# Performance work log

Measured on AMD Instinct MI355X. Metric: run time of the kernel, lower is better.

## Reference

```python
import jax, jax.numpy as jnp
import numpy as np

N = 50000       # nodes
E = 800000      # edges
IN_DIM = 256    # input_dim
HEADS = 4
CH = 32         # per-head channels (hidden_dim; conv3 uses latent_dim//heads = 32 too)
HC = HEADS * CH # 128
ED = 32         # edge_dims


def setup_inputs():
    key = jax.random.key(0)
    ks = iter(jax.random.split(key, 64))
    def nrm(shape):
        return jax.random.normal(next(ks), shape, dtype=jnp.float32) * 0.05
    inp = {}
    inp["x"] = nrm((N, IN_DIM))
    inp["edge_index"] = jax.random.randint(next(ks), (2, E), 0, N)
    inp["attr"] = nrm((E, ED))
    for l, ind in ((1, IN_DIM), (2, HC), (3, HC)):
        inp[f"Wq{l}"] = nrm((ind, HC)); inp[f"bq{l}"] = jnp.zeros((HC,), jnp.float32)
        inp[f"Wk{l}"] = nrm((ind, HC)); inp[f"bk{l}"] = jnp.zeros((HC,), jnp.float32)
        inp[f"Wv{l}"] = nrm((ind, HC)); inp[f"bv{l}"] = jnp.zeros((HC,), jnp.float32)
        inp[f"We{l}"] = nrm((ED, HC))  # lin_edge has no bias in PyG TransformerConv
        inp[f"Ws{l}"] = nrm((ind, HC)); inp[f"bs{l}"] = jnp.zeros((HC,), jnp.float32)
    inp["g1"] = jnp.ones((HC,), jnp.float32); inp["be1"] = jnp.zeros((HC,), jnp.float32)
    inp["g2"] = jnp.ones((HC,), jnp.float32); inp["be2"] = jnp.zeros((HC,), jnp.float32)
    return inp


def _transformer_conv(x, src, dst, attr, Wq, bq, Wk, bk, Wv, bv, We, Ws, bs):
    # PyG TransformerConv, concat=True, root_weight=True, beta=False, dropout=0 (eval).
    q = (x @ Wq + bq).reshape(-1, HEADS, CH)   # [N,H,C] (queries at dst)
    k = (x @ Wk + bk).reshape(-1, HEADS, CH)
    v = (x @ Wv + bv).reshape(-1, HEADS, CH)
    e = (attr @ We).reshape(-1, HEADS, CH)     # [E,H,C]
    kj = k[src] + e                            # edge-conditioned keys  [E,H,C]
    vj = v[src] + e                            # edge-conditioned values [E,H,C]
    alpha = jnp.einsum('ehc,ehc->eh', q[dst], kj) / np.sqrt(CH).astype(np.float32)
    # segment softmax over incoming edges per destination node, per head
    amax = jax.ops.segment_max(alpha, dst, num_segments=N)          # [N,H]
    amax = jnp.where(jnp.isfinite(amax), amax, 0.0)                 # nodes with no edges
    ex = jnp.exp(alpha - amax[dst])                                 # [E,H]
    den = jax.ops.segment_sum(ex, dst, num_segments=N)              # [N,H]
    a = ex / (den[dst] + 1e-16)                                     # [E,H]
    out = jax.ops.segment_sum(a[..., None] * vj, dst, num_segments=N)  # [N,H,C]
    out = out.reshape(-1, HC) + (x @ Ws + bs)                       # + root skip
    return out, a


def _layernorm(x, g, b):
    m = x.mean(-1, keepdims=True)
    v = x.var(-1, keepdims=True)
    return (x - m) / jnp.sqrt(v + 1e-5) * g + b


def reference(x, edge_index, attr,
              Wq1, bq1, Wk1, bk1, Wv1, bv1, We1, Ws1, bs1,
              Wq2, bq2, Wk2, bk2, Wv2, bv2, We2, Ws2, bs2,
              Wq3, bq3, Wk3, bk3, Wv3, bv3, We3, Ws3, bs3,
              g1, be1, g2, be2):
    src, dst = edge_index[0], edge_index[1]
    h, a1 = _transformer_conv(x, src, dst, attr, Wq1, bq1, Wk1, bk1, Wv1, bv1, We1, Ws1, bs1)
    h = jax.nn.relu(_layernorm(h, g1, be1))   # dropout is identity in eval
    h, a2 = _transformer_conv(h, src, dst, attr, Wq2, bq2, Wk2, bk2, Wv2, bv2, We2, Ws2, bs2)
    h = jax.nn.relu(_layernorm(h, g2, be2))
    h, a3 = _transformer_conv(h, src, dst, attr, Wq3, bq3, Wk3, bk3, Wv3, bv3, We3, Ws3, bs3)
    return (h, a1, a2, a3)
```

## Files before the change

kernel.cpp:

```cpp
#include <hip/hip_runtime.h>
#include <math.h>

#define N_NODES 50000
#define E_EDGES 800000
#define HC 128
#define ED 32
#define SCH 64
#define SCHSZ 782

typedef __attribute__((ext_vector_type(8))) short bf16x8;
typedef __attribute__((ext_vector_type(4))) float f32x4;
typedef unsigned short ushort_t;

__device__ __forceinline__ ushort_t f2bf(float f){
    unsigned u = __float_as_uint(f);
    return (ushort_t)((u + 0x7FFFu + ((u >> 16) & 1u)) >> 16);
}
__device__ __forceinline__ float bflo(unsigned u){ return __uint_as_float(u << 16); }
__device__ __forceinline__ float bfhi(unsigned u){ return __uint_as_float(u & 0xffff0000u); }

__device__ __forceinline__ int weidx(int c, int d){
    return c * 40 + (((((d >> 2) + ((c >> 3) & 7)) & 7)) << 2) + (d & 3);
}


__global__ void hist_kernel(const int* __restrict__ dst, int* __restrict__ cnt, int n_edges){
    int e = blockIdx.x * blockDim.x + threadIdx.x;
    if (e < n_edges) atomicAdd(&cnt[dst[e]], 1);
}

__global__ __launch_bounds__(256) void chunk_hist_kernel(const int* __restrict__ cnt,
                                                         int* __restrict__ chist){
    __shared__ int hist[64];
    const int t = threadIdx.x, b = blockIdx.x;
    if (t < 64) hist[t] = 0;
    __syncthreads();
    const int base = b * SCHSZ;
    const int lim = min(base + SCHSZ, N_NODES);
    for (int i = base + t; i < lim; i += 256){
        int d = cnt[i]; if (d > 63) d = 63;
        atomicAdd(&hist[d], 1);
    }
    __syncthreads();
    if (t < 64) chist[b * 64 + t] = hist[t];
}

__global__ __launch_bounds__(1024) void scan_sort_kernel(
    const int* __restrict__ cnt, int* __restrict__ rowptr,
    int* __restrict__ cursor, const int* __restrict__ chist, int* __restrict__ cbase)
{
    __shared__ int part[1024];
    __shared__ int ch[SCH * 64];
    __shared__ int binbase[64];
    const int t = threadIdx.x;
    const int CH = (N_NODES + 1023) / 1024;
    const int base = t * CH;
    int s = 0;
    for (int i = 0; i < CH; i++){
        int idx = base + i;
        if (idx < N_NODES) s += cnt[idx];
    }
    part[t] = s;
    __syncthreads();
    for (int off = 1; off < 1024; off <<= 1){
        int v = (t >= off) ? part[t - off] : 0;
        __syncthreads();
        part[t] += v;
        __syncthreads();
    }
    int off = (t == 0) ? 0 : part[t - 1];
    for (int i = 0; i < CH; i++){
        int idx = base + i;
        if (idx < N_NODES){
            int c = cnt[idx];
            rowptr[idx] = off;
            cursor[idx] = off;
            off += c;
        }
    }
    if (t == 1023) rowptr[N_NODES] = part[1023];

    for (int i = t; i < SCH * 64; i += 1024) ch[i] = chist[i];
    __syncthreads();
    if (t < 64){
        int tot = 0;
        for (int c = 0; c < SCH; c++) tot += ch[c * 64 + t];
        binbase[t] = tot;
    }
    __syncthreads();
    if (t == 0){
        int acc = 0;
        for (int b = 0; b < 64; b++){ int v = binbase[b]; binbase[b] = acc; acc += v; }
    }
    __syncthreads();
    for (int i = t; i < SCH * 64; i += 1024){
        int c = i >> 6, d = i & 63;
        int acc = binbase[d];
        for (int c2 = 0; c2 < c; c2++) acc += ch[c2 * 64 + d];
        cbase[i] = acc;
    }
}

__global__ __launch_bounds__(256) void scatter_kernel(
    const int* __restrict__ src, const int* __restrict__ dst,
    int* __restrict__ cursor, int2* __restrict__ es, int n_edges,
    const int* __restrict__ cnt, const int* __restrict__ cbase, int* __restrict__ norder)
{
    __shared__ int cur[64];
    const int b = blockIdx.x, t = threadIdx.x;
    const bool sorter = (b < SCH);
    if (sorter && t < 64) cur[t] = cbase[b * 64 + t];
    int e = b * 256 + t;
    if (e < n_edges){
        int d = dst[e];
        int pos = atomicAdd(&cursor[d], 1);
        es[pos] = make_int2(e, src[e]);
    }
    if (sorter){
        __syncthreads();
        const int base = b * SCHSZ;
        const int lim = min(base + SCHSZ, N_NODES);
        for (int i = base + t; i < lim; i += 256){
            int d = cnt[i]; if (d > 63) d = 63;
            int pos = atomicAdd(&cur[d], 1);
            norder[pos] = i;
        }
    }
}

__device__ __forceinline__ void pack_item(const float* __restrict__ Wq, const float* __restrict__ Wk,
                                          const float* __restrict__ Wv, const float* __restrict__ Ws,
                                          const float* __restrict__ We, ushort_t* __restrict__ Bp,
                                          int K, int item){
    int n = item % 640, k = item / 640;
    float val;
    if (n < 512){
        const float* W = (n < 128) ? Wq : (n < 256) ? Wk : (n < 384) ? Wv : Ws;
        val = W[k * HC + (n & 127)];
    } else {
        int col = n - 512, h5 = (col >> 5) * 32, d = col & 31;
        float acc = 0.f;
        for (int c = 0; c < 32; c++)
            acc = fmaf(Wq[k * HC + h5 + c], We[d * HC + h5 + c], acc);
        val = acc;
    }
    Bp[(((size_t)(k >> 3)) * 640 + n) * 8 + (k & 7)] = f2bf(val);
}

#define T_S0 12800000
#define T_S1 16000000
#define T_S2 16163840
#define T_S3 16245760
#define T_S4 16327680
#define T_S5 16328064

__global__ __launch_bounds__(256) void tail_kernel(
    const float* __restrict__ attr, const int2* __restrict__ es,
    const float* __restrict__ x, int perm_mode,
    ushort_t* __restrict__ attr_bf, ushort_t* __restrict__ Xbf,
    const float* __restrict__ Wq0, const float* __restrict__ bq0, const float* __restrict__ Wk0,
    const float* __restrict__ Wv0, const float* __restrict__ Ws0, const float* __restrict__ We0,
    const float* __restrict__ Wq1, const float* __restrict__ bq1, const float* __restrict__ Wk1,
    const float* __restrict__ Wv1, const float* __restrict__ Ws1, const float* __restrict__ We1,
    const float* __restrict__ Wq2, const float* __restrict__ bq2, const float* __restrict__ Wk2,
    const float* __restrict__ Wv2, const float* __restrict__ Ws2, const float* __restrict__ We2,
    ushort_t* __restrict__ Bp0, ushort_t* __restrict__ Bp1, ushort_t* __restrict__ Bp2,
    float* __restrict__ qwb3)
{
    const int stride = gridDim.x * blockDim.x;
    for (int gi = blockIdx.x * blockDim.x + threadIdx.x; gi < T_S5; gi += stride){
        if (gi < T_S0){
            if (perm_mode){
                int grp = gi >> 4, lane = gi & 15;
                int e = es[grp].x;
                const float2 v = *(const float2*)&attr[(size_t)e * ED + lane * 2];
                unsigned r = (unsigned)f2bf(v.x) | ((unsigned)f2bf(v.y) << 16);
                ((unsigned*)attr_bf)[(size_t)grp * (ED / 2) + lane] = r;
            }
        } else if (gi < T_S1){
            int i = gi - T_S0;
            float4 v = ((const float4*)x)[i];
            ushort_t r0 = f2bf(v.x), r1 = f2bf(v.y), r2 = f2bf(v.z), r3 = f2bf(v.w);
            ((ushort4*)Xbf)[i] = make_ushort4(r0, r1, r2, r3);
        } else if (gi < T_S2){
            pack_item(Wq0, Wk0, Wv0, Ws0, We0, Bp0, 256, gi - T_S1);
        } else if (gi < T_S3){
            pack_item(Wq1, Wk1, Wv1, Ws1, We1, Bp1, 128, gi - T_S2);
        } else if (gi < T_S4){
            pack_item(Wq2, Wk2, Wv2, Ws2, We2, Bp2, 128, gi - T_S3);
        } else {
            int f = gi - T_S4;
            int l = f >> 7, t2 = f & 127;
            const float* bq = (l == 0) ? bq0 : (l == 1) ? bq1 : bq2;
            const float* We = (l == 0) ? We0 : (l == 1) ? We1 : We2;
            int h5 = (t2 >> 5) * 32, d = t2 & 31;
            float acc = 0.f;
            for (int c = 0; c < 32; c++)
                acc = fmaf(bq[h5 + c], We[d * HC + h5 + c], acc);
            qwb3[l * HC + t2] = acc;
        }
    }
}

template<int K>
__global__ __launch_bounds__(320) void gemm_mfma(
    const ushort_t* __restrict__ Xbf, const ushort_t* __restrict__ Bpack,
    const float* __restrict__ b0, const float* __restrict__ b1,
    const float* __restrict__ b2, const float* __restrict__ b3,
    const float* __restrict__ b4,
    float* __restrict__ Yq, ushort_t* __restrict__ Ykbf,
    ushort_t* __restrict__ Yvbf, float* __restrict__ Ys,
    float* __restrict__ Yw, int M)
{
    const int w = threadIdx.x >> 6;
    const int lane = threadIdx.x & 63;
    const int q = lane >> 4, nn = lane & 15;
    const int row0 = blockIdx.x * 32;

    f32x4 acc[2][8];
    #pragma unroll
    for (int mt = 0; mt < 2; mt++)
        #pragma unroll
        for (int nt = 0; nt < 8; nt++)
            acc[mt][nt] = (f32x4){0.f, 0.f, 0.f, 0.f};

    const int r0 = row0 + nn;
    const int r1 = row0 + 16 + nn;
    const bf16x8 zf = (bf16x8){0,0,0,0,0,0,0,0};

    #pragma unroll
    for (int kc = 0; kc < K / 32; kc++){
        bf16x8 a0 = (r0 < M) ? *(const bf16x8*)&Xbf[(size_t)r0 * K + kc * 32 + q * 8] : zf;
        bf16x8 a1 = (r1 < M) ? *(const bf16x8*)&Xbf[(size_t)r1 * K + kc * 32 + q * 8] : zf;
        bf16x8 b[8];
        #pragma unroll
        for (int nt = 0; nt < 8; nt++){
            int n = w * 128 + nt * 16 + nn;
            b[nt] = *(const bf16x8*)&Bpack[(((size_t)(kc * 4 + q)) * 640 + n) * 8];
        }
        #pragma unroll
        for (int nt = 0; nt < 8; nt++){
            acc[0][nt] = __builtin_amdgcn_mfma_f32_16x16x32_bf16(a0, b[nt], acc[0][nt], 0, 0, 0);
            acc[1][nt] = __builtin_amdgcn_mfma_f32_16x16x32_bf16(a1, b[nt], acc[1][nt], 0, 0, 0);
        }
    }

    const float scale = (w == 0 || w == 4) ? 0.17677669529663687f : 1.f;
    const float* bias = (w == 0) ? b0 : (w == 1) ? b1 : (w == 2) ? b2 : (w == 3) ? b3 : b4;

    if (w == 1 || w == 2){
        ushort_t* Yb = (w == 1) ? Ykbf : Yvbf;
        #pragma unroll
        for (int nt = 0; nt < 8; nt++){
            int col = nt * 16 + nn;
            float bval = bias[col];
            #pragma unroll
            for (int mt = 0; mt < 2; mt++){
                #pragma unroll
                for (int r = 0; r < 4; r++){
                    int row = row0 + mt * 16 + q * 4 + r;
                    if (row < M) Yb[(size_t)row * HC + col] = f2bf(acc[mt][nt][r] + bval);
                }
            }
        }
    } else {
        float* Y = (w == 0) ? Yq : (w == 3) ? Ys : Yw;
        #pragma unroll
        for (int nt = 0; nt < 8; nt++){
            int col = nt * 16 + nn;
            float bval = bias[col];
            #pragma unroll
            for (int mt = 0; mt < 2; mt++){
                #pragma unroll
                for (int r = 0; r < 4; r++){
                    int row = row0 + mt * 16 + q * 4 + r;
                    if (row < M) Y[(size_t)row * HC + col] = (acc[mt][nt][r] + bval) * scale;
                }
            }
        }
    }
}

__device__ __forceinline__ float dot16s(const uint4 kk, const uint4 aa,
                                        const float4 qA, const float4 qB,
                                        const float4 wA, const float4 wB){
    float pa =            bflo(kk.x) * qA.x;
    pa = fmaf(bfhi(kk.x), qA.y, pa);
    pa = fmaf(bflo(kk.y), qA.z, pa);
    pa = fmaf(bfhi(kk.y), qA.w, pa);
    pa = fmaf(bflo(aa.x), wA.x, pa);
    pa = fmaf(bfhi(aa.x), wA.y, pa);
    pa = fmaf(bflo(aa.y), wA.z, pa);
    pa = fmaf(bfhi(aa.y), wA.w, pa);
    float pb =            bflo(kk.z) * qB.x;
    pb = fmaf(bfhi(kk.z), qB.y, pb);
    pb = fmaf(bflo(kk.w), qB.z, pb);
    pb = fmaf(bfhi(kk.w), qB.w, pb);
    pb = fmaf(bflo(aa.z), wB.x, pb);
    pb = fmaf(bfhi(aa.z), wB.y, pb);
    pb = fmaf(bflo(aa.w), wB.z, pb);
    pb = fmaf(bfhi(aa.w), wB.w, pb);
    return pa + pb;
}

__device__ __forceinline__ uint4 packrow(const float* p){
    float4 x = *(const float4*)p;
    float4 y = *(const float4*)(p + 4);
    uint4 r;
    r.x = (unsigned)f2bf(x.x) | ((unsigned)f2bf(x.y) << 16);
    r.y = (unsigned)f2bf(x.z) | ((unsigned)f2bf(x.w) << 16);
    r.z = (unsigned)f2bf(y.x) | ((unsigned)f2bf(y.y) << 16);
    r.w = (unsigned)f2bf(y.z) | ((unsigned)f2bf(y.w) << 16);
    return r;
}

__global__ __launch_bounds__(256) void fused_attn_kernel(
    const float* __restrict__ qs, const float* __restrict__ qw,
    const ushort_t* __restrict__ kb, const ushort_t* __restrict__ vb,
    const float* __restrict__ skip, const float* __restrict__ We,
    const float* __restrict__ attr, const ushort_t* __restrict__ attr_bf, int perm_mode,
    const int* __restrict__ rowptr, const int2* __restrict__ es,
    const int* __restrict__ norder,
    float* __restrict__ acsr, float* __restrict__ a_out,
    const float* __restrict__ g, const float* __restrict__ be,
    float* __restrict__ out_f32, ushort_t* __restrict__ out_bf, int apply_ln)
{
    __shared__ float WeT[5120];
    __shared__ float SL[2304];
    const int t = threadIdx.x;
    for (int idx = t; idx < ED * HC; idx += 256){
        int d = idx >> 7, c = idx & 127;
        WeT[weidx(c, d)] = We[idx];
    }
    __syncthreads();

    const int lane = t & 63, wvi = t >> 6;
    const int qq = lane >> 4, li = lane & 15;
    const int h = li >> 2, jj = li & 3;
    const int gq = blockIdx.x * 16 + wvi * 4 + qq;
    if (gq >= N_NODES) return;
    const int n = norder[gq];
    const int ch = h * 32 + jj * 8;
    const size_t nrow = (size_t)n * HC + ch;

    const float4 qA = *(const float4*)&qs[nrow];
    const float4 qB = *(const float4*)&qs[nrow + 4];
    const float4 wA = *(const float4*)&qw[nrow];
    const float4 wB = *(const float4*)&qw[nrow + 4];
    const float4 skA = *(const float4*)&skip[nrow];
    const float4 skB = *(const float4*)&skip[nrow + 4];

    const int beg = rowptr[n], end = rowptr[n + 1];
    float m = -1e30f, s = 0.f;
    float acc[8] = {0,0,0,0,0,0,0,0};
    float S[8]   = {0,0,0,0,0,0,0,0};

    for (int i = beg; i < end; i += 4){
        const int cnt = end - i;
        uint4 kk[4], vv[4], aa[4];
        #pragma unroll
        for (int b = 0; b < 4; b++){
            kk[b] = (uint4){0,0,0,0}; vv[b] = (uint4){0,0,0,0}; aa[b] = (uint4){0,0,0,0};
            if (b < cnt){
                const int2 e = es[i + b];
                kk[b] = *(const uint4*)&kb[(size_t)e.y * HC + ch];
                vv[b] = *(const uint4*)&vb[(size_t)e.y * HC + ch];
                if (perm_mode)
                    aa[b] = *(const uint4*)&attr_bf[(size_t)(i + b) * ED + jj * 8];
                else
                    aa[b] = packrow(&attr[(size_t)e.x * ED + jj * 8]);
            }
        }
        float al[4];
        #pragma unroll
        for (int b = 0; b < 4; b++){
            float p = dot16s(kk[b], aa[b], qA, qB, wA, wB);
            p += __shfl_xor(p, 1);
            p += __shfl_xor(p, 2);
            al[b] = (b < cnt) ? p : -1e38f;
        }
        if (jj == 0){
            #pragma unroll
            for (int b = 0; b < 4; b++)
                if (b < cnt) acsr[(size_t)(i + b) * 4 + h] = al[b];
        }
        const float mn = fmaxf(fmaxf(m, fmaxf(al[0], al[1])), fmaxf(al[2], al[3]));
        const float sc = __expf(m - mn);
        m = mn;
        const float w0 = __expf(al[0] - mn);
        const float w1 = __expf(al[1] - mn);
        const float w2 = __expf(al[2] - mn);
        const float w3 = __expf(al[3] - mn);
        s = fmaf(s, sc, (w0 + w1) + (w2 + w3));
        acc[0] = fmaf(acc[0], sc, fmaf(w0, bflo(vv[0].x), fmaf(w1, bflo(vv[1].x), fmaf(w2, bflo(vv[2].x), w3 * bflo(vv[3].x)))));
        acc[1] = fmaf(acc[1], sc, fmaf(w0, bfhi(vv[0].x), fmaf(w1, bfhi(vv[1].x), fmaf(w2, bfhi(vv[2].x), w3 * bfhi(vv[3].x)))));
        acc[2] = fmaf(acc[2], sc, fmaf(w0, bflo(vv[0].y), fmaf(w1, bflo(vv[1].y), fmaf(w2, bflo(vv[2].y), w3 * bflo(vv[3].y)))));
        acc[3] = fmaf(acc[3], sc, fmaf(w0, bfhi(vv[0].y), fmaf(w1, bfhi(vv[1].y), fmaf(w2, bfhi(vv[2].y), w3 * bfhi(vv[3].y)))));
        acc[4] = fmaf(acc[4], sc, fmaf(w0, bflo(vv[0].z), fmaf(w1, bflo(vv[1].z), fmaf(w2, bflo(vv[2].z), w3 * bflo(vv[3].z)))));
        acc[5] = fmaf(acc[5], sc, fmaf(w0, bfhi(vv[0].z), fmaf(w1, bfhi(vv[1].z), fmaf(w2, bfhi(vv[2].z), w3 * bfhi(vv[3].z)))));
        acc[6] = fmaf(acc[6], sc, fmaf(w0, bflo(vv[0].w), fmaf(w1, bflo(vv[1].w), fmaf(w2, bflo(vv[2].w), w3 * bflo(vv[3].w)))));
        acc[7] = fmaf(acc[7], sc, fmaf(w0, bfhi(vv[0].w), fmaf(w1, bfhi(vv[1].w), fmaf(w2, bfhi(vv[2].w), w3 * bfhi(vv[3].w)))));
        S[0] = fmaf(S[0], sc, fmaf(w0, bflo(aa[0].x), fmaf(w1, bflo(aa[1].x), fmaf(w2, bflo(aa[2].x), w3 * bflo(aa[3].x)))));
        S[1] = fmaf(S[1], sc, fmaf(w0, bfhi(aa[0].x), fmaf(w1, bfhi(aa[1].x), fmaf(w2, bfhi(aa[2].x), w3 * bfhi(aa[3].x)))));
        S[2] = fmaf(S[2], sc, fmaf(w0, bflo(aa[0].y), fmaf(w1, bflo(aa[1].y), fmaf(w2, bflo(aa[2].y), w3 * bflo(aa[3].y)))));
        S[3] = fmaf(S[3], sc, fmaf(w0, bfhi(aa[0].y), fmaf(w1, bfhi(aa[1].y), fmaf(w2, bfhi(aa[2].y), w3 * bfhi(aa[3].y)))));
        S[4] = fmaf(S[4], sc, fmaf(w0, bflo(aa[0].z), fmaf(w1, bflo(aa[1].z), fmaf(w2, bflo(aa[2].z), w3 * bflo(aa[3].z)))));
        S[5] = fmaf(S[5], sc, fmaf(w0, bfhi(aa[0].z), fmaf(w1, bfhi(aa[1].z), fmaf(w2, bfhi(aa[2].z), w3 * bfhi(aa[3].z)))));
        S[6] = fmaf(S[6], sc, fmaf(w0, bflo(aa[0].w), fmaf(w1, bflo(aa[1].w), fmaf(w2, bflo(aa[2].w), w3 * bflo(aa[3].w)))));
        S[7] = fmaf(S[7], sc, fmaf(w0, bfhi(aa[0].w), fmaf(w1, bfhi(aa[1].w), fmaf(w2, bfhi(aa[2].w), w3 * bfhi(aa[3].w)))));
    }

    const int nl = wvi * 4 + qq;
    const int sbase = nl * 144;
    const int hsk = h * 36;
    *(float4*)&SL[sbase + hsk + jj * 8]     = make_float4(S[0], S[1], S[2], S[3]);
    *(float4*)&SL[sbase + hsk + jj * 8 + 4] = make_float4(S[4], S[5], S[6], S[7]);
    asm volatile("" ::: "memory");
    float E[8] = {0,0,0,0,0,0,0,0};
    #pragma unroll
    for (int d4 = 0; d4 < 8; d4++){
        const float4 sv = *(const float4*)&SL[sbase + hsk + d4 * 4];
        #pragma unroll
        for (int r = 0; r < 8; r++){
            const float4 wv = *(const float4*)&WeT[weidx(ch + r, d4 * 4)];
            E[r] = fmaf(sv.x, wv.x, fmaf(sv.y, wv.y, fmaf(sv.z, wv.z, fmaf(sv.w, wv.w, E[r]))));
        }
    }

    const float inv = 1.f / (s + 1e-16f);
    float o[8];
    o[0] = (acc[0] + E[0]) * inv + skA.x;
    o[1] = (acc[1] + E[1]) * inv + skA.y;
    o[2] = (acc[2] + E[2]) * inv + skA.z;
    o[3] = (acc[3] + E[3]) * inv + skA.w;
    o[4] = (acc[4] + E[4]) * inv + skB.x;
    o[5] = (acc[5] + E[5]) * inv + skB.y;
    o[6] = (acc[6] + E[6]) * inv + skB.z;
    o[7] = (acc[7] + E[7]) * inv + skB.w;

    if (apply_ln){
        float s1 = 0.f, s2 = 0.f;
        #pragma unroll
        for (int r = 0; r < 8; r++){ s1 += o[r]; s2 = fmaf(o[r], o[r], s2); }
        #pragma unroll
        for (int off = 1; off <= 8; off <<= 1){
            s1 += __shfl_xor(s1, off);
            s2 += __shfl_xor(s2, off);
        }
        const float mu  = s1 * (1.f / 128.f);
        const float var = s2 * (1.f / 128.f) - mu * mu;
        const float ivs = rsqrtf(var + 1e-5f);
        const float4 gA = *(const float4*)&g[ch];
        const float4 gB = *(const float4*)&g[ch + 4];
        const float4 bA = *(const float4*)&be[ch];
        const float4 bB = *(const float4*)&be[ch + 4];
        o[0] = fmaxf((o[0] - mu) * ivs * gA.x + bA.x, 0.f);
        o[1] = fmaxf((o[1] - mu) * ivs * gA.y + bA.y, 0.f);
        o[2] = fmaxf((o[2] - mu) * ivs * gA.z + bA.z, 0.f);
        o[3] = fmaxf((o[3] - mu) * ivs * gA.w + bA.w, 0.f);
        o[4] = fmaxf((o[4] - mu) * ivs * gB.x + bB.x, 0.f);
        o[5] = fmaxf((o[5] - mu) * ivs * gB.y + bB.y, 0.f);
        o[6] = fmaxf((o[6] - mu) * ivs * gB.z + bB.z, 0.f);
        o[7] = fmaxf((o[7] - mu) * ivs * gB.w + bB.w, 0.f);
        uint4 st;
        st.x = (unsigned)f2bf(o[0]) | ((unsigned)f2bf(o[1]) << 16);
        st.y = (unsigned)f2bf(o[2]) | ((unsigned)f2bf(o[3]) << 16);
        st.z = (unsigned)f2bf(o[4]) | ((unsigned)f2bf(o[5]) << 16);
        st.w = (unsigned)f2bf(o[6]) | ((unsigned)f2bf(o[7]) << 16);
        *(uint4*)&out_bf[nrow] = st;
    } else {
        *(float4*)&out_f32[nrow]     = make_float4(o[0], o[1], o[2], o[3]);
        *(float4*)&out_f32[nrow + 4] = make_float4(o[4], o[5], o[6], o[7]);
    }

    const float mh = __shfl(m, (qq << 4) + ((li & 3) << 2));
    const float dh = __shfl(s, (qq << 4) + ((li & 3) << 2));
    const float ih = 1.f / (dh + 1e-16f);
    asm volatile("s_waitcnt vmcnt(0)" ::: "memory");
    for (int f = beg * 4 + li; f < end * 4; f += 16){
        const int e = es[f >> 2].x;
        a_out[(size_t)e * 4 + (li & 3)] = __expf(acsr[f] - mh) * ih;
    }
}


extern "C" void kernel_launch(void* const* d_in, const int* in_sizes, int n_in,
                              void* d_out, int out_size, void* d_ws, size_t ws_size,
                              hipStream_t stream) {
    const float* x    = (const float*)d_in[0];
    const int*   ei   = (const int*)  d_in[1];
    const float* attr = (const float*)d_in[2];
    const float* gln[2]  = { (const float*)d_in[30], (const float*)d_in[32] };
    const float* beln[2] = { (const float*)d_in[31], (const float*)d_in[33] };

    float* out   = (float*)d_out;
    float* h_out = out;
    float* a_out[3] = { out + (size_t)N_NODES * HC,
                        out + (size_t)N_NODES * HC + (size_t)E_EDGES * 4,
                        out + (size_t)N_NODES * HC + (size_t)2 * E_EDGES * 4 };

    char* base = (char*)d_ws;
    size_t off = 0;
    auto alloc = [&](size_t bytes) -> void* {
        void* p = base + off;
        off = (off + bytes + 63) & ~(size_t)63;
        return p;
    };
    const size_t NB = (size_t)N_NODES * HC;
    float* qbuf     = (float*)alloc(NB * 4);
    float* qwbuf    = (float*)alloc(NB * 4);
    ushort_t* kbf   = (ushort_t*)alloc(NB * 2);
    ushort_t* vbf   = (ushort_t*)alloc(NB * 2);
    float* sbuf     = (float*)alloc(NB * 4);
    int* rowptr     = (int*)alloc((N_NODES + 1) * 4);
    int* cnt        = (int*)alloc(N_NODES * 4);
    int* cursor     = (int*)alloc(N_NODES * 4);
    int* norder     = (int*)alloc(N_NODES * 4);
    int* chist      = (int*)alloc(SCH * 64 * 4);
    int* cbase      = (int*)alloc(SCH * 64 * 4);
    int2* es        = (int2*)alloc((size_t)E_EDGES * 8);
    ushort_t* Xbf   = (ushort_t*)alloc((size_t)N_NODES * 256 * 2);
    ushort_t* Hbf   = (ushort_t*)alloc(NB * 2);
    ushort_t* Bp0   = (ushort_t*)alloc((size_t)256 * 640 * 2);
    ushort_t* Bp1   = (ushort_t*)alloc((size_t)128 * 640 * 2);
    ushort_t* Bp2   = (ushort_t*)alloc((size_t)128 * 640 * 2);
    float* acsr     = (float*)alloc((size_t)E_EDGES * 4 * 4);
    float* qwb3     = (float*)alloc((size_t)3 * HC * 4);
    ushort_t* attr_bf = (ushort_t*)alloc((size_t)E_EDGES * ED * 2);
    const int perm_mode = (ws_size >= off) ? 1 : 0;

    const int* srcp = ei;
    const int* dstp = ei + E_EDGES;

    hipMemsetAsync(cnt, 0, (size_t)N_NODES * 4, stream);
    hist_kernel<<<(E_EDGES + 255) / 256, 256, 0, stream>>>(dstp, cnt, E_EDGES);
    chunk_hist_kernel<<<SCH, 256, 0, stream>>>(cnt, chist);
    scan_sort_kernel<<<1, 1024, 0, stream>>>(cnt, rowptr, cursor, chist, cbase);
    scatter_kernel<<<(E_EDGES + 255) / 256, 256, 0, stream>>>(
        srcp, dstp, cursor, es, E_EDGES, cnt, cbase, norder);
    tail_kernel<<<4096, 256, 0, stream>>>(
        attr, es, x, perm_mode, attr_bf, Xbf,
        (const float*)d_in[3],  (const float*)d_in[4],  (const float*)d_in[5],
        (const float*)d_in[7],  (const float*)d_in[10], (const float*)d_in[9],
        (const float*)d_in[12], (const float*)d_in[13], (const float*)d_in[14],
        (const float*)d_in[16], (const float*)d_in[19], (const float*)d_in[18],
        (const float*)d_in[21], (const float*)d_in[22], (const float*)d_in[23],
        (const float*)d_in[25], (const float*)d_in[28], (const float*)d_in[27],
        Bp0, Bp1, Bp2, qwb3);

    const int gemm_grid = (N_NODES + 31) / 32;
    const int attn_grid = (N_NODES + 15) / 16;
    ushort_t* Bps[3] = { Bp0, Bp1, Bp2 };

    for (int l = 0; l < 3; l++){
        const float* bq = (const float*)d_in[3 + 9 * l + 1];
        const float* bk = (const float*)d_in[3 + 9 * l + 3];
        const float* bv = (const float*)d_in[3 + 9 * l + 5];
        const float* We = (const float*)d_in[3 + 9 * l + 6];
        const float* bs = (const float*)d_in[3 + 9 * l + 8];

        if (l == 0)
            gemm_mfma<256><<<gemm_grid, 320, 0, stream>>>(Xbf, Bps[l], bq, bk, bv, bs, qwb3 + 128 * l,
                                                          qbuf, kbf, vbf, sbuf, qwbuf, N_NODES);
        else
            gemm_mfma<128><<<gemm_grid, 320, 0, stream>>>(Hbf, Bps[l], bq, bk, bv, bs, qwb3 + 128 * l,
                                                          qbuf, kbf, vbf, sbuf, qwbuf, N_NODES);

        const float* gg = (l < 2) ? gln[l] : nullptr;
        const float* bb = (l < 2) ? beln[l] : nullptr;
        fused_attn_kernel<<<attn_grid, 256, 0, stream>>>(
            qbuf, qwbuf, kbf, vbf, sbuf, We, attr, attr_bf, perm_mode,
            rowptr, es, norder, acsr, a_out[l], gg, bb,
            (l < 2) ? nullptr : h_out, (l < 2) ? Hbf : nullptr, (l < 2) ? 1 : 0);
    }
}
```

Baseline: 1.046 ms.

## Replace single-block CSR scan with chunked multi-block rowptr fill

The single 1024-thread block that scanned 50000 degree counts and computed the degree-bucket bases is removed. Chunk sums are now produced in chunk_hist_kernel, a 64-block kernel does a per-chunk scan to fill rowptr and cursor, and the bucket-base prefix is recomputed inside each sorter block of scatter_kernel. This targets the serial latency of a one-block scan in the CSR build, at the cost of extra shared-memory work and barriers in the scatter sorter blocks. The CSR build is a small share of the total time, so the effect should be modest.

```diff
diff --git a/kernel.cpp b/kernel.cpp
--- a/kernel.cpp
+++ b/kernel.cpp
@@ -30,86 +30,109 @@
 }
 
 __global__ __launch_bounds__(256) void chunk_hist_kernel(const int* __restrict__ cnt,
-                                                         int* __restrict__ chist){
+                                                         int* __restrict__ chist,
+                                                         int* __restrict__ csum){
     __shared__ int hist[64];
+    __shared__ int red[256];
     const int t = threadIdx.x, b = blockIdx.x;
     if (t < 64) hist[t] = 0;
     __syncthreads();
     const int base = b * SCHSZ;
     const int lim = min(base + SCHSZ, N_NODES);
+    int mysum = 0;
     for (int i = base + t; i < lim; i += 256){
-        int d = cnt[i]; if (d > 63) d = 63;
+        int d = cnt[i];
+        mysum += d;
+        if (d > 63) d = 63;
         atomicAdd(&hist[d], 1);
     }
+    red[t] = mysum;
     __syncthreads();
+    for (int off = 128; off; off >>= 1){
+        if (t < off) red[t] += red[t + off];
+        __syncthreads();
+    }
     if (t < 64) chist[b * 64 + t] = hist[t];
-}
-
-__global__ __launch_bounds__(1024) void scan_sort_kernel(
-    const int* __restrict__ cnt, int* __restrict__ rowptr,
-    int* __restrict__ cursor, const int* __restrict__ chist, int* __restrict__ cbase)
+    if (t == 0) csum[b] = red[0];
+}
+
+__global__ __launch_bounds__(256) void fill_rowptr_kernel(
+    const int* __restrict__ cnt, const int* __restrict__ csum,
+    int* __restrict__ rowptr, int* __restrict__ cursor)
 {
-    __shared__ int part[1024];
-    __shared__ int ch[SCH * 64];
-    __shared__ int binbase[64];
-    const int t = threadIdx.x;
-    const int CH = (N_NODES + 1023) / 1024;
-    const int base = t * CH;
-    int s = 0;
-    for (int i = 0; i < CH; i++){
-        int idx = base + i;
-        if (idx < N_NODES) s += cnt[idx];
-    }
-    part[t] = s;
-    __syncthreads();
-    for (int off = 1; off < 1024; off <<= 1){
-        int v = (t >= off) ? part[t - off] : 0;
-        __syncthreads();
-        part[t] += v;
-        __syncthreads();
-    }
-    int off = (t == 0) ? 0 : part[t - 1];
-    for (int i = 0; i < CH; i++){
-        int idx = base + i;
-        if (idx < N_NODES){
-            int c = cnt[idx];
-            rowptr[idx] = off;
-            cursor[idx] = off;
-            off += c;
-        }
-    }
-    if (t == 1023) rowptr[N_NODES] = part[1023];
-
-    for (int i = t; i < SCH * 64; i += 1024) ch[i] = chist[i];
-    __syncthreads();
-    if (t < 64){
-        int tot = 0;
-        for (int c = 0; c < SCH; c++) tot += ch[c * 64 + t];
-        binbase[t] = tot;
-    }
-    __syncthreads();
+    __shared__ int ts[256];
+    __shared__ int chunkbase;
+    const int b = blockIdx.x, t = threadIdx.x;
     if (t == 0){
         int acc = 0;
-        for (int b = 0; b < 64; b++){ int v = binbase[b]; binbase[b] = acc; acc += v; }
-    }
+        for (int c = 0; c < b; c++) acc += csum[c];
+        chunkbase = acc;
+    }
+    const int base = b * SCHSZ;
+    const int lim = min(base + SCHSZ, N_NODES);
+    const int idx0 = base + t * 4;
+    int c[4];
+    int local = 0;
+    #pragma unroll
+    for (int j = 0; j < 4; j++){
+        int idx = idx0 + j;
+        c[j] = (idx < lim) ? cnt[idx] : 0;
+        local += c[j];
+    }
+    ts[t] = local;
     __syncthreads();
-    for (int i = t; i < SCH * 64; i += 1024){
-        int c = i >> 6, d = i & 63;
-        int acc = binbase[d];
-        for (int c2 = 0; c2 < c; c2++) acc += ch[c2 * 64 + d];
-        cbase[i] = acc;
-    }
+    for (int off = 1; off < 256; off <<= 1){
+        int v = (t >= off) ? ts[t - off] : 0;
+        __syncthreads();
+        ts[t] += v;
+        __syncthreads();
+    }
+    int off0 = chunkbase + ((t == 0) ? 0 : ts[t - 1]);
+    #pragma unroll
+    for (int j = 0; j < 4; j++){
+        int idx = idx0 + j;
+        if (idx < lim){
+            rowptr[idx] = off0;
+            cursor[idx] = off0;
+            off0 += c[j];
+        }
+    }
+    if (b == SCH - 1 && t == 255) rowptr[N_NODES] = chunkbase + ts[255];
 }
 
 __global__ __launch_bounds__(256) void scatter_kernel(
     const int* __restrict__ src, const int* __restrict__ dst,
     int* __restrict__ cursor, int2* __restrict__ es, int n_edges,
-    const int* __restrict__ cnt, const int* __restrict__ cbase, int* __restrict__ norder)
+    const int* __restrict__ cnt, const int* __restrict__ chist, int* __restrict__ norder)
 {
+    __shared__ int chs[SCH * 64];
+    __shared__ int bt[64];
+    __shared__ int bb[64];
     __shared__ int cur[64];
     const int b = blockIdx.x, t = threadIdx.x;
     const bool sorter = (b < SCH);
-    if (sorter && t < 64) cur[t] = cbase[b * 64 + t];
+    int pre = 0;
+    if (sorter){
+        for (int i = t; i < SCH * 64; i += 256) chs[i] = chist[i];
+        __syncthreads();
+        if (t < 64){
+            int tot = 0;
+            for (int c = 0; c < SCH; c++){
+                int v = chs[c * 64 + t];
+                tot += v;
+                if (c < b) pre += v;
+            }
+            bt[t] = tot;
+        }
+        __syncthreads();
+        if (t == 0){
+            int a = 0;
+            for (int d = 0; d < 64; d++){ int v = bt[d]; bb[d] = a; a += v; }
+        }
+        __syncthreads();
+        if (t < 64) cur[t] = bb[t] + pre;
+        __syncthreads();
+    }
     int e = b * 256 + t;
     if (e < n_edges){
         int d = dst[e];
@@ -117,7 +140,6 @@
         es[pos] = make_int2(e, src[e]);
     }
     if (sorter){
-        __syncthreads();
         const int base = b * SCHSZ;
         const int lim = min(base + SCHSZ, N_NODES);
         for (int i = base + t; i < lim; i += 256){
@@ -517,7 +539,7 @@
     int* cursor     = (int*)alloc(N_NODES * 4);
     int* norder     = (int*)alloc(N_NODES * 4);
     int* chist      = (int*)alloc(SCH * 64 * 4);
-    int* cbase      = (int*)alloc(SCH * 64 * 4);
+    int* csum       = (int*)alloc(SCH * 4);
     int2* es        = (int2*)alloc((size_t)E_EDGES * 8);
     ushort_t* Xbf   = (ushort_t*)alloc((size_t)N_NODES * 256 * 2);
     ushort_t* Hbf   = (ushort_t*)alloc(NB * 2);
@@ -534,10 +556,10 @@
 
     hipMemsetAsync(cnt, 0, (size_t)N_NODES * 4, stream);
     hist_kernel<<<(E_EDGES + 255) / 256, 256, 0, stream>>>(dstp, cnt, E_EDGES);
-    chunk_hist_kernel<<<SCH, 256, 0, stream>>>(cnt, chist);
-    scan_sort_kernel<<<1, 1024, 0, stream>>>(cnt, rowptr, cursor, chist, cbase);
+    chunk_hist_kernel<<<SCH, 256, 0, stream>>>(cnt, chist, csum);
+    fill_rowptr_kernel<<<SCH, 256, 0, stream>>>(cnt, csum, rowptr, cursor);
     scatter_kernel<<<(E_EDGES + 255) / 256, 256, 0, stream>>>(
-        srcp, dstp, cursor, es, E_EDGES, cnt, cbase, norder);
+        srcp, dstp, cursor, es, E_EDGES, cnt, chist, norder);
     tail_kernel<<<4096, 256, 0, stream>>>(
         attr, es, x, perm_mode, attr_bf, Xbf,
         (const float*)d_in[3],  (const float*)d_in[4],  (const float*)d_in[5],
```

Measured after the change: 921.4 us, median of 2. 11.9% less time.
